# Performance work log

Measured on AMD Instinct MI355X. Metric: run time of the kernel, lower is better.

## Reference

```python
import jax, jax.numpy as jnp
import numpy as np

R = 8          # shuffle_rate
HEADS = 4
DIM_HEAD = 64


def setup_inputs() -> dict:
    key = jax.random.key(0)
    k1, k2, k3 = jax.random.split(key, 3)
    dim = 64
    C = dim * R * R            # 4096, token channel dim after unshuffle
    inner = HEADS * DIM_HEAD   # 256
    x = jax.random.normal(k1, (8, dim, 256, 256), dtype=jnp.float32)
    W_qkv = jax.random.normal(k2, (C, 3 * inner), dtype=jnp.float32) * (C ** -0.5)
    W_out = jax.random.normal(k3, (inner, C), dtype=jnp.float32) * (inner ** -0.5)
    b_out = jnp.zeros((C,), dtype=jnp.float32)
    return {"x": x, "W_qkv": W_qkv, "W_out": W_out, "b_out": b_out}


def reference(x, W_qkv, W_out, b_out):
    scale = DIM_HEAD ** -0.5
    B, C0, H0, W0 = x.shape
    h, w = H0 // R, W0 // R
    N = h * w
    C = C0 * R * R
    # PixelUnshuffle: [B,C0,H0,W0] -> [B, C0*R*R, h, w]
    xd = x.reshape(B, C0, h, R, w, R).transpose(0, 1, 3, 5, 2, 4).reshape(B, C, h, w)
    # flatten spatial -> tokens [B, N, C]
    tokens = xd.reshape(B, C, N).transpose(0, 2, 1)
    qkv = tokens @ W_qkv                                   # [B, N, 3*inner]
    q, k, v = jnp.split(qkv, 3, axis=-1)
    def heads(t):  # [B,N,inner] -> [B,H,N,d]
        return t.reshape(B, N, HEADS, DIM_HEAD).transpose(0, 2, 1, 3)
    q, k, v = heads(q), heads(k), heads(v)
    dots = jnp.einsum('bhnd,bhmd->bhnm', q, k) * scale
    attn = jax.nn.softmax(dots, axis=-1)
    out = jnp.einsum('bhnm,bhmd->bhnd', attn, v)
    out = out.transpose(0, 2, 1, 3).reshape(B, N, HEADS * DIM_HEAD)
    y = out @ W_out + b_out                                # [B, N, C]
    y = y.transpose(0, 2, 1).reshape(B, C, h, w)
    # PixelShuffle: [B, C0*R*R, h, w] -> [B, C0, H0, W0]
    y = y.reshape(B, C0, R, R, h, w).transpose(0, 1, 4, 2, 5, 3).reshape(B, C0, H0, W0)
    return y
```

## Files before the change

### kernel.cpp

```cpp
#include <hip/hip_runtime.h>

typedef unsigned short u16;
typedef __attribute__((ext_vector_type(8))) short s16x8;
typedef __attribute__((ext_vector_type(4))) short s16x4;
typedef __attribute__((ext_vector_type(4))) float f32x4;

__device__ __forceinline__ u16 f2bf(float f) {
    unsigned int u;
    __builtin_memcpy(&u, &f, 4);
    unsigned int r = u + 0x7FFFu + ((u >> 16) & 1u);
    return (u16)(r >> 16);
}

__device__ __forceinline__ void gl_lds16(const u16* g, u16* l) {
    __builtin_amdgcn_global_load_lds(
        (const __attribute__((address_space(1))) unsigned int*)g,
        (__attribute__((address_space(3))) unsigned int*)l,
        16, 0, 0);
}

__global__ __launch_bounds__(256) void k_unshuffle(const float* __restrict__ x,
                                                   u16* __restrict__ tok) {
    int idx = blockIdx.x * 256 + threadIdx.x;
    int r1  = idx & 7;
    int xxg = (idx >> 3) & 7;
    int yy  = (idx >> 6) & 31;
    int c0  = (idx >> 11) & 63;
    int b   = idx >> 17;

    const float* src = x + ((size_t)((b * 64 + c0) * 256 + yy * 8 + r1)) * 256 + xxg * 32;
    int mbase = b * 1024 + yy * 32 + xxg * 4;
    int cbase = c0 * 64 + r1 * 8;
    for (int q = 0; q < 4; ++q) {
        float4 f0 = *(const float4*)(src + q * 8);
        float4 f1 = *(const float4*)(src + q * 8 + 4);
        s16x8 v;
        v[0] = (short)f2bf(f0.x); v[1] = (short)f2bf(f0.y);
        v[2] = (short)f2bf(f0.z); v[3] = (short)f2bf(f0.w);
        v[4] = (short)f2bf(f1.x); v[5] = (short)f2bf(f1.y);
        v[6] = (short)f2bf(f1.z); v[7] = (short)f2bf(f1.w);
        *(s16x8*)(tok + (size_t)(mbase + q) * 4096 + cbase) = v;
    }
}

__global__ __launch_bounds__(256) void k_transpose(const float* __restrict__ in,
                                                   u16* __restrict__ out,
                                                   int rows, int cols) {
    __shared__ float tile[64][65];
    int bx = blockIdx.x * 64, by = blockIdx.y * 64;
    int tx = threadIdx.x & 63, ty = threadIdx.x >> 6;
    for (int i = ty; i < 64; i += 4)
        tile[i][tx] = in[(size_t)(by + i) * cols + bx + tx];
    __syncthreads();
    for (int i = ty; i < 64; i += 4)
        out[(size_t)(bx + i) * rows + by + tx] = f2bf(tile[tx][i]);
}

__global__ __launch_bounds__(256) void k_gemm_qkv(const u16* __restrict__ A,
                                                  const u16* __restrict__ Bt,
                                                  float* __restrict__ P) {
    const int K = 4096;
    __shared__ u16 As[128 * 64];
    __shared__ u16 Bs[128 * 64];
    const int tid = threadIdx.x;
    const int wave = tid >> 6, lane = tid & 63;
    const int quad = lane >> 4, l15 = lane & 15;
    const int wm = wave >> 1, wn = wave & 1;
    const int tm = blockIdx.y * 128, tn = blockIdx.x * 128;
    const int z = blockIdx.z;

    f32x4 acc[4][4] = {};

    for (int k0 = z * 2048; k0 < (z + 1) * 2048; k0 += 64) {
        __syncthreads();
        for (int t = 0; t < 4; ++t) {
            int c = wave * 256 + t * 64 + lane;
            int row = c >> 3, kc = c & 7;
            gl_lds16(A + (size_t)(tm + row) * K + k0 + kc * 8,
                     As + (wave * 256 + t * 64) * 8);
        }
        for (int t = 0; t < 4; ++t) {
            int c = wave * 256 + t * 64 + lane;
            int row = c >> 3, kc = c & 7;
            gl_lds16(Bt + (size_t)(tn + row) * K + k0 + kc * 8,
                     Bs + (wave * 256 + t * 64) * 8);
        }
        __syncthreads();
        for (int kk = 0; kk < 64; kk += 32) {
            s16x8 af[4], bf[4];
            for (int i = 0; i < 4; ++i)
                af[i] = *(const s16x8*)(As + (wm * 64 + i * 16 + l15) * 64 + kk + quad * 8);
            for (int j = 0; j < 4; ++j)
                bf[j] = *(const s16x8*)(Bs + (wn * 64 + j * 16 + l15) * 64 + kk + quad * 8);
            for (int i = 0; i < 4; ++i)
                for (int j = 0; j < 4; ++j)
                    acc[i][j] = __builtin_amdgcn_mfma_f32_16x16x32_bf16(af[i], bf[j], acc[i][j], 0, 0, 0);
        }
    }

    float* Pz = P + (size_t)z * 8192 * 768;
    for (int i = 0; i < 4; ++i) {
        int mb = tm + wm * 64 + i * 16 + quad * 4;
        for (int j = 0; j < 4; ++j) {
            int col = tn + wn * 64 + j * 16 + l15;
            for (int r = 0; r < 4; ++r)
                Pz[(size_t)(mb + r) * 768 + col] = acc[i][j][r];
        }
    }
}

__global__ __launch_bounds__(256) void k_qkv_reduce(const float* __restrict__ P,
                                                    u16* __restrict__ Qo,
                                                    u16* __restrict__ Ko,
                                                    u16* __restrict__ Vo) {
    int col = blockIdx.x * 256 + threadIdx.x;
    int m   = blockIdx.y;
    float v = P[(size_t)m * 768 + col] + P[(size_t)(8192 * 768) + (size_t)m * 768 + col];
    int which = col >> 8, h = (col >> 6) & 3, d = col & 63;
    int b = m >> 10, n = m & 1023;
    u16* dst = (which == 0) ? Qo : (which == 1) ? Ko : Vo;
    dst[((size_t)((b * 4 + h) * 1024 + n)) * 64 + d] = f2bf(v);
}

__global__ __launch_bounds__(256) void k_attn(const u16* __restrict__ Qb,
                                              const u16* __restrict__ Kb,
                                              const u16* __restrict__ Vb,
                                              u16* __restrict__ aout) {
    const int bh = blockIdx.y;
    const int q0 = blockIdx.x * 64;
    const int tid = threadIdx.x;
    const int wave = tid >> 6, lane = tid & 63;
    const int quad = lane >> 4, l15 = lane & 15;
    const size_t base = (size_t)bh * 1024 * 64;
    const float scale = 0.125f;

    __shared__ u16 Ks[64 * 64];
    __shared__ u16 Vts[64 * 68];
    __shared__ u16 Ps[4][16 * 64];

    s16x8 aq0, aq1;
    {
        const u16* qp = Qb + base + (size_t)(q0 + wave * 16 + l15) * 64 + quad * 8;
        aq0 = *(const s16x8*)(qp);
        aq1 = *(const s16x8*)(qp + 32);
    }

    float m_i[4], l_i[4];
    f32x4 o[4] = {};
    for (int r = 0; r < 4; ++r) { m_i[r] = -1e30f; l_i[r] = 0.f; }

    for (int t = 0; t < 16; ++t) {
        __syncthreads();
        for (int e = 0; e < 2; ++e) {
            int s = e * 256 + tid;
            int row = s >> 3, off = (s & 7) * 8;
            *(s16x8*)(Ks + row * 64 + off) =
                *(const s16x8*)(Kb + base + (size_t)(t * 64 + row) * 64 + off);
        }
        for (int e = 0; e < 16; ++e) {
            int s = e * 256 + tid;
            int kv = s >> 6, d = s & 63;
            Vts[d * 68 + kv] = Vb[base + (size_t)(t * 64 + kv) * 64 + d];
        }
        __syncthreads();

        f32x4 s4[4];
        for (int j = 0; j < 4; ++j) {
            const u16* kr = Ks + (j * 16 + l15) * 64 + quad * 8;
            s16x8 b0 = *(const s16x8*)(kr);
            s16x8 b1 = *(const s16x8*)(kr + 32);
            f32x4 c = {};
            c = __builtin_amdgcn_mfma_f32_16x16x32_bf16(aq0, b0, c, 0, 0, 0);
            c = __builtin_amdgcn_mfma_f32_16x16x32_bf16(aq1, b1, c, 0, 0, 0);
            s4[j] = c;
        }

        for (int r = 0; r < 4; ++r) {
            float sv0 = s4[0][r] * scale, sv1 = s4[1][r] * scale;
            float sv2 = s4[2][r] * scale, sv3 = s4[3][r] * scale;
            float mt = fmaxf(fmaxf(sv0, sv1), fmaxf(sv2, sv3));
            for (int off = 1; off < 16; off <<= 1)
                mt = fmaxf(mt, __shfl_xor(mt, off, 64));
            float mn = fmaxf(m_i[r], mt);
            float alpha = __expf(m_i[r] - mn);
            m_i[r] = mn;
            float p0 = __expf(sv0 - mn), p1 = __expf(sv1 - mn);
            float p2 = __expf(sv2 - mn), p3 = __expf(sv3 - mn);
            u16* pw = Ps[wave] + (quad * 4 + r) * 64 + l15;
            pw[0]  = f2bf(p0);
            pw[16] = f2bf(p1);
            pw[32] = f2bf(p2);
            pw[48] = f2bf(p3);
            float rs = p0 + p1 + p2 + p3;
            for (int off = 1; off < 16; off <<= 1)
                rs += __shfl_xor(rs, off, 64);
            l_i[r] = l_i[r] * alpha + rs;
            for (int dt = 0; dt < 4; ++dt) o[dt][r] *= alpha;
        }

        for (int kk = 0; kk < 64; kk += 32) {
            s16x8 pf = *(const s16x8*)(Ps[wave] + l15 * 64 + kk + quad * 8);
            for (int dt = 0; dt < 4; ++dt) {
                const u16* vr = Vts + (dt * 16 + l15) * 68 + kk + quad * 8;
                s16x4 v0 = *(const s16x4*)(vr);
                s16x4 v1 = *(const s16x4*)(vr + 4);
                s16x8 vf;
                vf[0] = v0[0]; vf[1] = v0[1]; vf[2] = v0[2]; vf[3] = v0[3];
                vf[4] = v1[0]; vf[5] = v1[1]; vf[6] = v1[2]; vf[7] = v1[3];
                o[dt] = __builtin_amdgcn_mfma_f32_16x16x32_bf16(pf, vf, o[dt], 0, 0, 0);
            }
        }
    }

    int b = bh >> 2, h = bh & 3;
    for (int dt = 0; dt < 4; ++dt)
        for (int r = 0; r < 4; ++r) {
            int qrow = q0 + wave * 16 + quad * 4 + r;
            float val = o[dt][r] / l_i[r];
            aout[((size_t)(b) * 1024 + qrow) * 256 + h * 64 + dt * 16 + l15] = f2bf(val);
        }
}

__global__ __launch_bounds__(256) void k_gemm_out(const u16* __restrict__ A,
                                                  const u16* __restrict__ Bt,
                                                  const float* __restrict__ bias,
                                                  float* __restrict__ out) {
    const int K = 256;
    __shared__ u16 As[128 * 64];
    __shared__ u16 Bs[128 * 64];
    const int tid = threadIdx.x;
    const int wave = tid >> 6, lane = tid & 63;
    const int quad = lane >> 4, l15 = lane & 15;
    const int wm = wave >> 1, wn = wave & 1;
    const int tm = blockIdx.y * 128, tn = blockIdx.x * 128;

    f32x4 acc[4][4] = {};

    for (int k0 = 0; k0 < K; k0 += 64) {
        __syncthreads();
        for (int t = 0; t < 4; ++t) {
            int c = wave * 256 + t * 64 + lane;
            int row = c >> 3, kc = c & 7;
            gl_lds16(A + (size_t)(tm + row) * K + k0 + kc * 8,
                     As + (wave * 256 + t * 64) * 8);
        }
        for (int t = 0; t < 4; ++t) {
            int c = wave * 256 + t * 64 + lane;
            int row = c >> 3, kc = c & 7;
            gl_lds16(Bt + (size_t)(tn + row) * K + k0 + kc * 8,
                     Bs + (wave * 256 + t * 64) * 8);
        }
        __syncthreads();
        for (int kk = 0; kk < 64; kk += 32) {
            s16x8 af[4], bf[4];
            for (int i = 0; i < 4; ++i)
                af[i] = *(const s16x8*)(As + (wm * 64 + i * 16 + l15) * 64 + kk + quad * 8);
            for (int j = 0; j < 4; ++j)
                bf[j] = *(const s16x8*)(Bs + (wn * 64 + j * 16 + l15) * 64 + kk + quad * 8);
            for (int i = 0; i < 4; ++i)
                for (int j = 0; j < 4; ++j)
                    acc[i][j] = __builtin_amdgcn_mfma_f32_16x16x32_bf16(af[i], bf[j], acc[i][j], 0, 0, 0);
        }
    }

    for (int i = 0; i < 4; ++i) {
        int mb = tm + wm * 64 + i * 16 + quad * 4;
        for (int j = 0; j < 4; ++j) {
            int col = tn + wn * 64 + j * 16 + l15;
            float bb = bias[col];
            int c0 = col >> 6, r1 = (col >> 3) & 7, r2 = col & 7;
            for (int r = 0; r < 4; ++r) {
                int m = mb + r;
                int b = m >> 10, n = m & 1023, yy = n >> 5, xx = n & 31;
                size_t oidx = ((size_t)((b * 64 + c0) * 256 + yy * 8 + r1)) * 256 + xx * 8 + r2;
                out[oidx] = acc[i][j][r] + bb;
            }
        }
    }
}

extern "C" void kernel_launch(void* const* d_in, const int* in_sizes, int n_in,
                              void* d_out, int out_size, void* d_ws, size_t ws_size,
                              hipStream_t stream) {
    (void)in_sizes; (void)n_in; (void)out_size; (void)ws_size;
    const float* x    = (const float*)d_in[0];
    const float* Wqkv = (const float*)d_in[1];
    const float* Wout = (const float*)d_in[2];
    const float* bout = (const float*)d_in[3];
    float* out = (float*)d_out;

    u16* ws     = (u16*)d_ws;
    u16* tokens = ws;
    u16* wqkvT  = tokens + 33554432;
    u16* woutT  = wqkvT + 3145728;
    u16* Qb     = woutT + 1048576;
    u16* Kb     = Qb + 2097152;
    u16* Vb     = Kb + 2097152;
    u16* aoutb  = Vb + 2097152;
    float* Pp   = (float*)(aoutb + 2097152);

    k_unshuffle<<<4096, 256, 0, stream>>>(x, tokens);
    k_transpose<<<dim3(12, 64), 256, 0, stream>>>(Wqkv, wqkvT, 4096, 768);
    k_transpose<<<dim3(64, 4), 256, 0, stream>>>(Wout, woutT, 256, 4096);
    k_gemm_qkv<<<dim3(6, 64, 2), 256, 0, stream>>>(tokens, wqkvT, Pp);
    k_qkv_reduce<<<dim3(3, 8192), 256, 0, stream>>>(Pp, Qb, Kb, Vb);
    k_attn<<<dim3(16, 32), 256, 0, stream>>>(Qb, Kb, Vb, aoutb);
    k_gemm_out<<<dim3(32, 64), 256, 0, stream>>>(aoutb, woutT, bout, out);
}
```

Before: 428.5 us.

## Store V pre-transposed in reduce kernel and vectorize attention K/V tile loads

The QKV reduce kernel now writes V in a transposed [b,h,d,n] layout using an LDS tile transpose, so the attention kernel can load V tiles with 16-byte vector loads instead of scalar transposing gathers. K tiles are loaded with direct global-to-LDS copies, and the final normalization uses a reciprocal multiply. This targets the scattered scalar V loads in the attention inner loop, at the cost of extra shared-memory traffic and a sync in the reduce kernel.

```diff
diff --git a/kernel.cpp b/kernel.cpp
--- a/kernel.cpp
+++ b/kernel.cpp
@@ -112,19 +112,46 @@
 __global__ __launch_bounds__(256) void k_qkv_reduce(const float* __restrict__ P,
                                                     u16* __restrict__ Qo,
                                                     u16* __restrict__ Ko,
-                                                    u16* __restrict__ Vo) {
-    int col = blockIdx.x * 256 + threadIdx.x;
-    int m   = blockIdx.y;
-    float v = P[(size_t)m * 768 + col] + P[(size_t)(8192 * 768) + (size_t)m * 768 + col];
-    int which = col >> 8, h = (col >> 6) & 3, d = col & 63;
-    int b = m >> 10, n = m & 1023;
-    u16* dst = (which == 0) ? Qo : (which == 1) ? Ko : Vo;
-    dst[((size_t)((b * 4 + h) * 1024 + n)) * 64 + d] = f2bf(v);
+                                                    u16* __restrict__ Vt) {
+    __shared__ u16 tile[64][65];
+    const int tid = threadIdx.x;
+    const int ct = blockIdx.x, mt = blockIdx.y;
+    const int c_l = tid & 63;
+    const int col = ct * 64 + c_l;
+    const int mbase = mt * 64;
+    const float* P1 = P + (size_t)8192 * 768;
+
+    if (ct < 8) {
+        int which = col >> 8;
+        int h = (col >> 6) & 3, d = col & 63;
+        u16* dst = (which == 0) ? Qo : Ko;
+        for (int k = 0; k < 16; ++k) {
+            int m = mbase + (tid >> 6) + k * 4;
+            float v = P[(size_t)m * 768 + col] + P1[(size_t)m * 768 + col];
+            int b = m >> 10, n = m & 1023;
+            dst[((size_t)((b * 4 + h) * 1024 + n)) * 64 + d] = f2bf(v);
+        }
+    } else {
+        int h = ct - 8;
+        int b = mbase >> 10;
+        int nbase = mbase & 1023;
+        for (int k = 0; k < 16; ++k) {
+            int ml = (tid >> 6) + k * 4;
+            int m = mbase + ml;
+            float v = P[(size_t)m * 768 + col] + P1[(size_t)m * 768 + col];
+            tile[ml][c_l] = f2bf(v);
+        }
+        __syncthreads();
+        for (int k = 0; k < 16; ++k) {
+            int d = (tid >> 6) + k * 4;
+            Vt[((size_t)((b * 4 + h) * 64 + d)) * 1024 + nbase + c_l] = tile[c_l][d];
+        }
+    }
 }
 
 __global__ __launch_bounds__(256) void k_attn(const u16* __restrict__ Qb,
                                               const u16* __restrict__ Kb,
-                                              const u16* __restrict__ Vb,
+                                              const u16* __restrict__ Vt,
                                               u16* __restrict__ aout) {
     const int bh = blockIdx.y;
     const int q0 = blockIdx.x * 64;
@@ -149,18 +176,20 @@
     f32x4 o[4] = {};
     for (int r = 0; r < 4; ++r) { m_i[r] = -1e30f; l_i[r] = 0.f; }
 
+    const int vrow = tid >> 2, vpart = tid & 3;
+
     for (int t = 0; t < 16; ++t) {
         __syncthreads();
         for (int e = 0; e < 2; ++e) {
             int s = e * 256 + tid;
-            int row = s >> 3, off = (s & 7) * 8;
-            *(s16x8*)(Ks + row * 64 + off) =
-                *(const s16x8*)(Kb + base + (size_t)(t * 64 + row) * 64 + off);
-        }
-        for (int e = 0; e < 16; ++e) {
-            int s = e * 256 + tid;
-            int kv = s >> 6, d = s & 63;
-            Vts[d * 68 + kv] = Vb[base + (size_t)(t * 64 + kv) * 64 + d];
+            gl_lds16(Kb + base + (size_t)t * 4096 + s * 8, Ks + s * 8);
+        }
+        {
+            const u16* src = Vt + base + (size_t)vrow * 1024 + t * 64 + vpart * 16;
+            s16x8 a = *(const s16x8*)(src);
+            s16x8 b2 = *(const s16x8*)(src + 8);
+            *(s16x8*)(Vts + vrow * 68 + vpart * 16) = a;
+            *(s16x8*)(Vts + vrow * 68 + vpart * 16 + 8) = b2;
         }
         __syncthreads();
 
@@ -213,11 +242,13 @@
     }
 
     int b = bh >> 2, h = bh & 3;
+    float rl[4];
+    for (int r = 0; r < 4; ++r) rl[r] = 1.0f / l_i[r];
     for (int dt = 0; dt < 4; ++dt)
         for (int r = 0; r < 4; ++r) {
             int qrow = q0 + wave * 16 + quad * 4 + r;
-            float val = o[dt][r] / l_i[r];
-            aout[((size_t)(b) * 1024 + qrow) * 256 + h * 64 + dt * 16 + l15] = f2bf(val);
+            aout[((size_t)(b) * 1024 + qrow) * 256 + h * 64 + dt * 16 + l15] =
+                f2bf(o[dt][r] * rl[r]);
         }
 }
 
@@ -295,15 +326,15 @@
     u16* woutT  = wqkvT + 3145728;
     u16* Qb     = woutT + 1048576;
     u16* Kb     = Qb + 2097152;
-    u16* Vb     = Kb + 2097152;
-    u16* aoutb  = Vb + 2097152;
+    u16* Vtb    = Kb + 2097152;
+    u16* aoutb  = Vtb + 2097152;
     float* Pp   = (float*)(aoutb + 2097152);
 
     k_unshuffle<<<4096, 256, 0, stream>>>(x, tokens);
     k_transpose<<<dim3(12, 64), 256, 0, stream>>>(Wqkv, wqkvT, 4096, 768);
     k_transpose<<<dim3(64, 4), 256, 0, stream>>>(Wout, woutT, 256, 4096);
     k_gemm_qkv<<<dim3(6, 64, 2), 256, 0, stream>>>(tokens, wqkvT, Pp);
-    k_qkv_reduce<<<dim3(3, 8192), 256, 0, stream>>>(Pp, Qb, Kb, Vb);
-    k_attn<<<dim3(16, 32), 256, 0, stream>>>(Qb, Kb, Vb, aoutb);
+    k_qkv_reduce<<<dim3(12, 128), 256, 0, stream>>>(Pp, Qb, Kb, Vtb);
+    k_attn<<<dim3(16, 32), 256, 0, stream>>>(Qb, Kb, Vtb, aoutb);
     k_gemm_out<<<dim3(32, 64), 256, 0, stream>>>(aoutb, woutT, bout, out);
 }
```

After: 422.1 us. About the same (-1.5%).
